# Kernel tuning notes

Hardware: AMD Instinct MI355X
Metric: run time of the kernel (lower is better)

## Reference

```python
import jax, jax.numpy as jnp
import numpy as np

MAX_CHILD = 64  # max trie branching factor (padding width for per-row child windows)


def setup_inputs() -> dict:
    key = jax.random.key(0)
    B, D, V, N = 1024, 1024, 32000, 200000
    k1, k2, k3, k4 = jax.random.split(key, 4)
    x = jax.random.normal(k1, (B, D), dtype=jnp.float32)
    weight = jax.random.normal(k2, (V, D), dtype=jnp.float32) * 0.02
    bias = jax.random.normal(k3, (V,), dtype=jnp.float32) * 0.02
    # Build a consistent CompactCSRTrie: offsets [N+1], tokens/child_nodes [E]
    rng = np.random.default_rng(0)
    deg = rng.integers(1, MAX_CHILD + 1, size=N)
    offsets = np.zeros(N + 1, dtype=np.int32)
    offsets[1:] = np.cumsum(deg)
    E = int(offsets[-1])
    tokens = rng.integers(0, V, size=E).astype(np.int32)
    child_nodes = rng.integers(0, N, size=E).astype(np.int32)
    cur_node = jax.random.randint(k4, (B,), 0, N, dtype=jnp.int32)
    return {
        "x": x,
        "weight": weight,
        "bias": bias,
        "cur_node": cur_node,
        "offsets": jnp.asarray(offsets),
        "tokens": jnp.asarray(tokens),
        "child_nodes": jnp.asarray(child_nodes),
        "step": 1,
    }


def reference(x, weight, bias, cur_node, offsets, tokens, child_nodes, step):
    # Dense GEMM part of the fused kernel: logits = x @ W^T + b  -> [B, V]
    logits = jnp.einsum("bd,vd->bv", x, weight) + bias
    B, V = logits.shape

    # CSR trie traversal: per row, the children of cur_node are
    # tokens[offsets[cur]:offsets[cur+1]] (valid next tokens) and
    # child_nodes[...] (next trie nodes). Gather a padded MAX_CHILD window.
    start = offsets[cur_node]                              # [B]
    deg = offsets[cur_node + 1] - start                    # [B]
    pos = jnp.arange(MAX_CHILD, dtype=start.dtype)         # [C]
    idx = jnp.minimum(start[:, None] + pos[None, :], tokens.shape[0] - 1)  # [B, C]
    valid = pos[None, :] < deg[:, None]                    # [B, C] bool

    tok = tokens[idx]                                      # [B, C] valid token columns
    child = child_nodes[idx]                               # [B, C] next trie nodes

    # Validity masking: only valid child tokens keep their logit, rest -> -inf
    rows = jnp.arange(B)[:, None]
    mask = jnp.zeros((B, V), dtype=bool).at[rows, tok].max(valid)
    masked_logits = jnp.where(mask, logits, -jnp.inf)

    next_nodes = jnp.where(valid, child, -1)               # [B, C], -1 padded
    valid_idxs = jnp.where(valid, tok, -1)                 # [B, C], -1 padded
    return next_nodes, valid_idxs, masked_logits
```

## Files before the change

### kernel.cpp

```cpp
#include <hip/hip_runtime.h>
#include <math.h>

#define B_ 1024
#define D_ 1024
#define V_ 32000
#define MAXC 64
#define BLOCK 1024

#define NEG_FILL (-3.0e38f)

typedef float vfloat4 __attribute__((ext_vector_type(4)));

__global__ __launch_bounds__(BLOCK, 4) void constrained_linear_kernel(
    const float* __restrict__ x,
    const float* __restrict__ weight,
    const float* __restrict__ bias,
    const int* __restrict__ cur_node,
    const int* __restrict__ offsets,
    const int* __restrict__ tokens,
    const int* __restrict__ child_nodes,
    float* __restrict__ next_nodes,
    float* __restrict__ valid_idxs,
    float* __restrict__ masked_logits)
{
    const int b = blockIdx.x;
    const int tid = threadIdx.x;
    const int wave = tid >> 6;
    const int lane = tid & 63;

    const int cur = cur_node[b];
    const int start = offsets[cur];
    int deg = offsets[cur + 1] - start;
    if (deg > MAXC) deg = MAXC;

    const float4* x4 = reinterpret_cast<const float4*>(x + (size_t)b * D_);
    float4 xv[4];
    #pragma unroll
    for (int k = 0; k < 4; ++k)
        xv[k] = x4[k * 64 + lane];

    float4 wv[4][4];
    float bj[4];
    int   tk[4];
    #pragma unroll
    for (int j = 0; j < 4; ++j) {
        const int c = wave + 16 * j;
        if (c < deg) {
            const int e = start + c;
            const int t = tokens[e];
            tk[j] = t;
            bj[j] = bias[t];
            const float4* w4 = reinterpret_cast<const float4*>(weight + (size_t)t * D_);
            #pragma unroll
            for (int k = 0; k < 4; ++k)
                wv[j][k] = w4[k * 64 + lane];
        }
    }

    if (tid < MAXC) {
        float nn = -1.0f, vi = -1.0f;
        if (tid < deg) {
            const int e = start + tid;
            nn = (float)child_nodes[e];
            vi = (float)tokens[e];
        }
        next_nodes[b * MAXC + tid] = nn;
        valid_idxs[b * MAXC + tid] = vi;
    }

    float* ml_row = masked_logits + (size_t)b * V_;
    vfloat4* ml4 = reinterpret_cast<vfloat4*>(ml_row);
    const vfloat4 sent = {NEG_FILL, NEG_FILL, NEG_FILL, NEG_FILL};
    #pragma unroll 2
    for (int i = tid; i < V_ / 4; i += BLOCK)
        __builtin_nontemporal_store(sent, &ml4[i]);

    float accs[4];
    #pragma unroll
    for (int j = 0; j < 4; ++j) {
        const int c = wave + 16 * j;
        if (c < deg) {
            float acc = 0.0f;
            #pragma unroll
            for (int k = 0; k < 4; ++k)
                acc += wv[j][k].x * xv[k].x + wv[j][k].y * xv[k].y +
                       wv[j][k].z * xv[k].z + wv[j][k].w * xv[k].w;
            #pragma unroll
            for (int off = 32; off > 0; off >>= 1)
                acc += __shfl_xor(acc, off);
            accs[j] = acc + bj[j];
        }
    }

    __syncthreads();

    #pragma unroll
    for (int j = 0; j < 4; ++j) {
        const int c = wave + 16 * j;
        if (c < deg && lane == 0)
            ml_row[tk[j]] = accs[j];
    }
}

extern "C" void kernel_launch(void* const* d_in, const int* in_sizes, int n_in,
                              void* d_out, int out_size, void* d_ws, size_t ws_size,
                              hipStream_t stream) {
    const float* x           = (const float*)d_in[0];
    const float* weight      = (const float*)d_in[1];
    const float* bias        = (const float*)d_in[2];
    const int*   cur_node    = (const int*)d_in[3];
    const int*   offsets     = (const int*)d_in[4];
    const int*   tokens      = (const int*)d_in[5];
    const int*   child_nodes = (const int*)d_in[6];

    float* out = (float*)d_out;
    float* next_nodes    = out;
    float* valid_idxs    = out + (size_t)B_ * MAXC;
    float* masked_logits = out + 2 * (size_t)B_ * MAXC;

    constrained_linear_kernel<<<B_, BLOCK, 0, stream>>>(
        x, weight, bias, cur_node, offsets, tokens, child_nodes,
        next_nodes, valid_idxs, masked_logits);
}
```

Measured before the change: 47.73 us.

## Split row into four 256-thread blocks and move scatter to second kernel

Each row's work is now split across four 256-thread blocks, each filling a quarter of the masked-logit row and computing 16 child dot products. This replaces one 1024-thread block per row and removes the intra-block barrier that serialized the fill and the scatter. The computed logits are staged in the next_nodes output region. A second kernel scatters them into the filled row and then overwrites that region with next_nodes and valid_idxs. The cost is an extra kernel launch and a round trip through global memory for the staged values.

```diff
diff --git a/kernel.cpp b/kernel.cpp
--- a/kernel.cpp
+++ b/kernel.cpp
@@ -5,25 +5,23 @@
 #define D_ 1024
 #define V_ 32000
 #define MAXC 64
-#define BLOCK 1024
 
 #define NEG_FILL (-3.0e38f)
 
 typedef float vfloat4 __attribute__((ext_vector_type(4)));
 
-__global__ __launch_bounds__(BLOCK, 4) void constrained_linear_kernel(
+__global__ __launch_bounds__(256, 4) void fill_compute_kernel(
     const float* __restrict__ x,
     const float* __restrict__ weight,
     const float* __restrict__ bias,
     const int* __restrict__ cur_node,
     const int* __restrict__ offsets,
     const int* __restrict__ tokens,
-    const int* __restrict__ child_nodes,
-    float* __restrict__ next_nodes,
-    float* __restrict__ valid_idxs,
-    float* __restrict__ masked_logits)
+    float* __restrict__ out)
 {
-    const int b = blockIdx.x;
+    const int bid = blockIdx.x;
+    const int b = bid >> 2;
+    const int q = bid & 3;
     const int tid = threadIdx.x;
     const int wave = tid >> 6;
     const int lane = tid & 63;
@@ -41,14 +39,11 @@
 
     float4 wv[4][4];
     float bj[4];
-    int   tk[4];
     #pragma unroll
     for (int j = 0; j < 4; ++j) {
-        const int c = wave + 16 * j;
+        const int c = q * 16 + wave * 4 + j;
         if (c < deg) {
-            const int e = start + c;
-            const int t = tokens[e];
-            tk[j] = t;
+            const int t = tokens[start + c];
             bj[j] = bias[t];
             const float4* w4 = reinterpret_cast<const float4*>(weight + (size_t)t * D_);
             #pragma unroll
@@ -57,28 +52,17 @@
         }
     }
 
-    if (tid < MAXC) {
-        float nn = -1.0f, vi = -1.0f;
-        if (tid < deg) {
-            const int e = start + tid;
-            nn = (float)child_nodes[e];
-            vi = (float)tokens[e];
-        }
-        next_nodes[b * MAXC + tid] = nn;
-        valid_idxs[b * MAXC + tid] = vi;
-    }
-
-    float* ml_row = masked_logits + (size_t)b * V_;
-    vfloat4* ml4 = reinterpret_cast<vfloat4*>(ml_row);
+    vfloat4* ml4 = reinterpret_cast<vfloat4*>(out + 2 * (size_t)B_ * MAXC + (size_t)b * V_);
     const vfloat4 sent = {NEG_FILL, NEG_FILL, NEG_FILL, NEG_FILL};
+    const int qbase = q * (V_ / 16);
     #pragma unroll 2
-    for (int i = tid; i < V_ / 4; i += BLOCK)
+    for (int i = qbase + tid; i < qbase + V_ / 16; i += 256)
         __builtin_nontemporal_store(sent, &ml4[i]);
 
-    float accs[4];
+    float* vals = out;
     #pragma unroll
     for (int j = 0; j < 4; ++j) {
-        const int c = wave + 16 * j;
+        const int c = q * 16 + wave * 4 + j;
         if (c < deg) {
             float acc = 0.0f;
             #pragma unroll
@@ -88,18 +72,39 @@
             #pragma unroll
             for (int off = 32; off > 0; off >>= 1)
                 acc += __shfl_xor(acc, off);
-            accs[j] = acc + bj[j];
+            if (lane == 0)
+                vals[b * MAXC + c] = acc + bj[j];
         }
     }
+}
 
-    __syncthreads();
+__global__ __launch_bounds__(256) void scatter_kernel(
+    const int* __restrict__ cur_node,
+    const int* __restrict__ offsets,
+    const int* __restrict__ tokens,
+    const int* __restrict__ child_nodes,
+    float* __restrict__ out)
+{
+    const int gid = blockIdx.x * 256 + threadIdx.x;
+    const int b = gid >> 6;
+    const int c = gid & (MAXC - 1);
 
-    #pragma unroll
-    for (int j = 0; j < 4; ++j) {
-        const int c = wave + 16 * j;
-        if (c < deg && lane == 0)
-            ml_row[tk[j]] = accs[j];
+    const int cur = cur_node[b];
+    const int start = offsets[cur];
+    int deg = offsets[cur + 1] - start;
+    if (deg > MAXC) deg = MAXC;
+
+    float nn = -1.0f, vi = -1.0f;
+    if (c < deg) {
+        const int e = start + c;
+        const int tok = tokens[e];
+        const float val = out[gid];
+        out[2 * (size_t)B_ * MAXC + (size_t)b * V_ + tok] = val;
+        nn = (float)child_nodes[e];
+        vi = (float)tok;
     }
+    out[gid] = nn;
+    out[(size_t)B_ * MAXC + gid] = vi;
 }
 
 extern "C" void kernel_launch(void* const* d_in, const int* in_sizes, int n_in,
@@ -114,11 +119,9 @@
     const int*   child_nodes = (const int*)d_in[6];
 
     float* out = (float*)d_out;
-    float* next_nodes    = out;
-    float* valid_idxs    = out + (size_t)B_ * MAXC;
-    float* masked_logits = out + 2 * (size_t)B_ * MAXC;
 
-    constrained_linear_kernel<<<B_, BLOCK, 0, stream>>>(
-        x, weight, bias, cur_node, offsets, tokens, child_nodes,
-        next_nodes, valid_idxs, masked_logits);
+    fill_compute_kernel<<<B_ * 4, 256, 0, stream>>>(
+        x, weight, bias, cur_node, offsets, tokens, out);
+    scatter_kernel<<<(B_ * MAXC) / 256, 256, 0, stream>>>(
+        cur_node, offsets, tokens, child_nodes, out);
 }
```

Measured after the change: 54.41 us. 1.14x slower.
